# Optimization experiments

Hardware: AMD Instinct MI355X
Metric: run time of the kernel (lower is better)

## Reference

```python
import jax, jax.numpy as jnp
import numpy as np

K = 7          # involution kernel size
G = 16         # groups = channels // group_channels = 256 // 16
BN_EPS = 1e-3  # Keras BatchNormalization default epsilon


def setup_inputs() -> dict:
    key = jax.random.key(0)
    ks = jax.random.split(key, 6)
    B, H, W, C = 4, 56, 56, 256
    Cr = C // 4                      # reduction_ratio = 4
    x = jax.random.normal(ks[0], (B, H, W, C), dtype=jnp.float32)
    w_reduce = jax.random.normal(ks[1], (C, Cr), dtype=jnp.float32) * (1.0 / np.sqrt(C))
    gamma = jnp.ones((Cr,), dtype=jnp.float32)
    beta = jnp.zeros((Cr,), dtype=jnp.float32)
    mean = jax.random.normal(ks[2], (Cr,), dtype=jnp.float32) * 0.1
    var = jax.random.uniform(ks[3], (Cr,), dtype=jnp.float32) + 0.5
    w_span = jax.random.normal(ks[4], (Cr, K * K * G), dtype=jnp.float32) * (1.0 / np.sqrt(Cr))
    b_span = jnp.zeros((K * K * G,), dtype=jnp.float32)
    return {"x": x, "w_reduce": w_reduce, "gamma": gamma, "beta": beta,
            "mean": mean, "var": var, "w_span": w_span, "b_span": b_span}


def reference(x, w_reduce, gamma, beta, mean, var, w_span, b_span):
    B, H, W, C = x.shape
    Cg = C // G  # channels per group
    # kernel generation branch: 1x1 conv -> BN (inference) -> ReLU -> 1x1 conv
    r = jnp.einsum('bhwc,cd->bhwd', x, w_reduce)
    r = jax.nn.relu((r - mean) * (gamma / jnp.sqrt(var + BN_EPS)) + beta)
    kgen = jnp.einsum('bhwd,de->bhwe', r, w_span) + b_span      # (B,H,W,K*K*G)
    kgen = kgen.reshape(B, H, W, G, K * K)
    # im2col with SAME padding (stride=1, pad (K-1)//2 symmetric), depth order (kh, kw, C)
    p = (K - 1) // 2
    xp = jnp.pad(x, ((0, 0), (p, p), (p, p), (0, 0)))
    patches = jnp.stack([xp[:, i:i + H, j:j + W, :]
                         for i in range(K) for j in range(K)], axis=3)  # (B,H,W,K*K,C)
    patches = patches.reshape(B, H, W, K * K, G, Cg)
    # per-pixel, per-group weighted reduction over the K*K window
    out = jnp.einsum('bhwgk,bhwkgc->bhwgc', kgen, patches)
    return out.reshape(B, H, W, C)
```

## Files before the change

### kernel.cpp

```cpp
#include <hip/hip_runtime.h>
#include <hip/hip_bf16.h>
#include <stdint.h>

#define B_   4
#define H_   56
#define W_   56
#define C_   256
#define CR   64
#define G_   16
#define CG   16
#define KS   7
#define KK   49
#define PADR 3
#define NPX  (B_*H_*W_)

typedef __attribute__((ext_vector_type(8))) short bf16x8;
typedef __attribute__((ext_vector_type(4))) float f32x4;
typedef __attribute__((ext_vector_type(2))) float f32x2;

__device__ __forceinline__ uint32_t f2bf(float f) {
    uint32_t x = __float_as_uint(f);
    return (x + 0x7fffu + ((x >> 16) & 1u)) >> 16;
}
__device__ __forceinline__ uint32_t pkbf(float a, float b) {
    union { __hip_bfloat162 h; uint32_t u; } c;
    c.h = __float22bfloat162_rn(make_float2(a, b));
    return c.u;
}
__device__ __forceinline__ float blo(uint32_t w) { return __uint_as_float(w << 16); }
__device__ __forceinline__ float bhi(uint32_t w) { return __uint_as_float(w & 0xffff0000u); }

union U4V { uint4 u; bf16x8 v; };

__global__ __launch_bounds__(256) void k0_prepack(
        const float* __restrict__ wr, const float* __restrict__ wspan,
        const float* __restrict__ gamma, const float* __restrict__ beta,
        const float* __restrict__ mean, const float* __restrict__ var,
        uint16_t* __restrict__ wrp, uint16_t* __restrict__ wpp,
        float* __restrict__ scale, float* __restrict__ shift) {
    int idx = blockIdx.x * 256 + threadIdx.x;
    {
        int j = idx & 7, lane = (idx >> 3) & 63, nb = (idx >> 9) & 3,
            kb = (idx >> 11) & 1, g = idx >> 12;
        int k = kb * 32 + (lane >> 4) * 8 + j;
        int n = nb * 16 + (lane & 15);
        float v = (n < KK) ? wspan[k * (KK * G_) + g * KK + n] : 0.f;
        wpp[idx] = (uint16_t)f2bf(v);
    }
    if (idx < 16384) {
        int j = idx & 7, lane = (idx >> 3) & 63, nb = (idx >> 9) & 3, kb = idx >> 11;
        int k = kb * 32 + (lane >> 4) * 8 + j;
        int n = nb * 16 + (lane & 15);
        wrp[idx] = (uint16_t)f2bf(wr[k * CR + n]);
    }
    if (idx < CR) {
        float s = gamma[idx] * rsqrtf(var[idx] + 1e-3f);
        scale[idx] = s;
        shift[idx] = beta[idx] - mean[idx] * s;
    }
}

__global__ __launch_bounds__(256) void k1_reduce(
        const float* __restrict__ x, const uint16_t* __restrict__ wrp,
        const float* __restrict__ scale, const float* __restrict__ shift,
        uint16_t* __restrict__ r) {
    int tid = threadIdx.x;
    int lane = tid & 63, w = tid >> 6;
    int mt = blockIdx.x * 4 + w;
    int pix = mt * 16 + (lane & 15);
    int ko = (lane >> 4) * 8;
    const float* xrow = x + (size_t)pix * C_ + ko;

    float s4[4], sh4[4];
    #pragma unroll
    for (int nb = 0; nb < 4; ++nb) {
        int d = nb * 16 + (lane & 15);
        s4[nb] = scale[d];
        sh4[nb] = shift[d];
    }

    float4 a0[8], a1[8];
    #pragma unroll
    for (int kb = 0; kb < 8; ++kb) {
        a0[kb] = *(const float4*)(xrow + kb * 32);
        a1[kb] = *(const float4*)(xrow + kb * 32 + 4);
    }
    f32x4 acc[4] = {{0,0,0,0},{0,0,0,0},{0,0,0,0},{0,0,0,0}};
    #pragma unroll
    for (int kb = 0; kb < 8; ++kb) {
        U4V af;
        af.u = make_uint4(pkbf(a0[kb].x, a0[kb].y), pkbf(a0[kb].z, a0[kb].w),
                          pkbf(a1[kb].x, a1[kb].y), pkbf(a1[kb].z, a1[kb].w));
        const uint16_t* wb = wrp + kb * 2048 + lane * 8;
        #pragma unroll
        for (int nb = 0; nb < 4; ++nb) {
            bf16x8 bf_ = *(const bf16x8*)(wb + nb * 512);
            acc[nb] = __builtin_amdgcn_mfma_f32_16x16x32_bf16(af.v, bf_, acc[nb], 0, 0, 0);
        }
    }
    int rq = (lane >> 4) * 4;
    #pragma unroll
    for (int nb = 0; nb < 4; ++nb) {
        #pragma unroll
        for (int rg = 0; rg < 4; ++rg) {
            float v = fmaf(acc[nb][rg], s4[nb], sh4[nb]);
            v = v > 0.f ? v : 0.f;
            r[(size_t)(mt * 16 + rq + rg) * CR + (nb * 16 + (lane & 15))] = (uint16_t)f2bf(v);
        }
    }
}

#define TS   14
#define HS   20
#define XSP  21
#define KGW  56

__global__ __launch_bounds__(256, 4) void k2_involution(
        const float* __restrict__ x, const uint16_t* __restrict__ r,
        const uint16_t* __restrict__ wpp, const float* __restrict__ bspan,
        float* __restrict__ out) {
    __shared__ __align__(16) uint16_t xs[420 * 16];
    __shared__ __align__(16) uint16_t kg[196 * KGW];

    int tid  = threadIdx.x;
    int tile = blockIdx.x, g = blockIdx.y, b = blockIdx.z;
    int ty0 = (tile >> 2) * TS, tx0 = (tile & 3) * TS;
    int lane = tid & 63, w = tid >> 6;

    bf16x8 bfr[2][4];
    const uint16_t* wb = wpp + g * 4096 + lane * 8;
    #pragma unroll
    for (int kb = 0; kb < 2; ++kb)
        #pragma unroll
        for (int nb = 0; nb < 4; ++nb)
            bfr[kb][nb] = *(const bf16x8*)(wb + kb * 2048 + nb * 512);
    float bias[4];
    #pragma unroll
    for (int nb = 0; nb < 4; ++nb) {
        int n = nb * 16 + (lane & 15);
        bias[nb] = (n < KK) ? bspan[g * KK + n] : 0.f;
    }

    #pragma unroll
    for (int pass = 0; pass < 2; ++pass) {
        int i = tid + pass * 256;
        if (i < HS * HS) {
            int py = i / HS, px = i % HS;
            int gy = ty0 + py - PADR, gx = tx0 + px - PADR;
            uint4 wA = make_uint4(0, 0, 0, 0), wB = wA;
            if (gy >= 0 && gy < H_ && gx >= 0 && gx < W_) {
                const float* xp = x + (((size_t)(b * H_ + gy)) * W_ + gx) * C_ + g * CG;
                float4 q0 = *(const float4*)(xp);
                float4 q1 = *(const float4*)(xp + 4);
                float4 q2 = *(const float4*)(xp + 8);
                float4 q3 = *(const float4*)(xp + 12);
                wA = make_uint4(pkbf(q0.x, q0.y), pkbf(q0.z, q0.w),
                                pkbf(q1.x, q1.y), pkbf(q1.z, q1.w));
                wB = make_uint4(pkbf(q2.x, q2.y), pkbf(q2.z, q2.w),
                                pkbf(q3.x, q3.y), pkbf(q3.z, q3.w));
            }
            uint16_t* dst = xs + (py * XSP + px) * 16;
            *(uint4*)(dst + 0) = wA;
            *(uint4*)(dst + 8) = wB;
        }
    }

    bf16x8 ra[4][2];
    #pragma unroll
    for (int mi = 0; mi < 4; ++mi) {
        int mt = mi * 4 + w;
        int mtc = mt < 13 ? mt : 12;
        int m  = mtc * 16 + (lane & 15);
        int mm = m < 196 ? m : 195;
        int ly = mm / TS, lx = mm % TS;
        size_t pix = ((size_t)(b * H_ + ty0 + ly)) * W_ + (tx0 + lx);
        const uint16_t* rp = r + pix * CR + (lane >> 4) * 8;
        ra[mi][0] = *(const bf16x8*)(rp);
        ra[mi][1] = *(const bf16x8*)(rp + 32);
    }
    #pragma unroll
    for (int mi = 0; mi < 4; ++mi) {
        int mt = mi * 4 + w;
        if (mt < 13) {
            f32x4 acc[4];
            #pragma unroll
            for (int nb = 0; nb < 4; ++nb)
                acc[nb] = (f32x4){bias[nb], bias[nb], bias[nb], bias[nb]};
            #pragma unroll
            for (int nb = 0; nb < 4; ++nb) {
                acc[nb] = __builtin_amdgcn_mfma_f32_16x16x32_bf16(ra[mi][0], bfr[0][nb], acc[nb], 0, 0, 0);
                acc[nb] = __builtin_amdgcn_mfma_f32_16x16x32_bf16(ra[mi][1], bfr[1][nb], acc[nb], 0, 0, 0);
            }
            int row = mt * 16 + (lane >> 4) * 4;
            if (row < 196) {
                #pragma unroll
                for (int nb = 0; nb < 4; ++nb) {
                    int n = nb * 16 + (lane & 15);
                    if (n < KK) {
                        int slot = n + n / 7;
                        #pragma unroll
                        for (int rg = 0; rg < 4; ++rg) {
                            int rr  = row + rg;
                            int rho = (rr >> 1) + (rr & 1) * 98;
                            kg[rho * KGW + slot] = (uint16_t)f2bf(acc[nb][rg]);
                        }
                    }
                }
            }
        }
    }
    __syncthreads();

    if (tid < 196) {
        int p = tid >> 1, h = tid & 1;
        int ty = p / 7, tx = (p % 7) * 2;
        const uint16_t* kgL = kg + p * KGW;
        const uint16_t* kgR = kg + (98 + p) * KGW;

        f32x2 accL[4] = {{0,0},{0,0},{0,0},{0,0}};
        f32x2 accR[4] = {{0,0},{0,0},{0,0},{0,0}};
        #pragma unroll
        for (int kh = 0; kh < KS; ++kh) {
            uint4 aL = *(const uint4*)(kgL + kh * 8);
            uint4 aR = *(const uint4*)(kgR + kh * 8);
            const uint32_t kwL[4] = {aL.x, aL.y, aL.z, aL.w};
            const uint32_t kwR[4] = {aR.x, aR.y, aR.z, aR.w};
            const uint16_t* xrow = xs + ((ty + kh) * XSP + tx) * 16 + h * 8;
            #pragma unroll
            for (int j = 0; j < 8; ++j) {
                uint4 xw = *(const uint4*)(xrow + j * 16);
                float kvL = 0.f, kvR = 0.f;
                if (j < 7) kvL = (j & 1) ? bhi(kwL[j >> 1]) : blo(kwL[j >> 1]);
                if (j > 0) { int t = j - 1; kvR = (t & 1) ? bhi(kwR[t >> 1]) : blo(kwR[t >> 1]); }
                f32x2 kL = {kvL, kvL}, kR = {kvR, kvR};
                f32x2 x0 = {blo(xw.x), bhi(xw.x)};
                f32x2 x1 = {blo(xw.y), bhi(xw.y)};
                f32x2 x2 = {blo(xw.z), bhi(xw.z)};
                f32x2 x3 = {blo(xw.w), bhi(xw.w)};
                accL[0] = __builtin_elementwise_fma(kL, x0, accL[0]);
                accL[1] = __builtin_elementwise_fma(kL, x1, accL[1]);
                accL[2] = __builtin_elementwise_fma(kL, x2, accL[2]);
                accL[3] = __builtin_elementwise_fma(kL, x3, accL[3]);
                accR[0] = __builtin_elementwise_fma(kR, x0, accR[0]);
                accR[1] = __builtin_elementwise_fma(kR, x1, accR[1]);
                accR[2] = __builtin_elementwise_fma(kR, x2, accR[2]);
                accR[3] = __builtin_elementwise_fma(kR, x3, accR[3]);
            }
        }
        size_t pixL = ((size_t)(b * H_ + ty0 + ty)) * W_ + (tx0 + tx);
        float* opL = out + pixL * C_ + g * CG + h * 8;
        float* opR = opL + C_;
        *(float4*)(opL + 0) = make_float4(accL[0].x, accL[0].y, accL[1].x, accL[1].y);
        *(float4*)(opL + 4) = make_float4(accL[2].x, accL[2].y, accL[3].x, accL[3].y);
        *(float4*)(opR + 0) = make_float4(accR[0].x, accR[0].y, accR[1].x, accR[1].y);
        *(float4*)(opR + 4) = make_float4(accR[2].x, accR[2].y, accR[3].x, accR[3].y);
    }
}

extern "C" void kernel_launch(void* const* d_in, const int* in_sizes, int n_in,
                              void* d_out, int out_size, void* d_ws, size_t ws_size,
                              hipStream_t stream) {
    const float* x        = (const float*)d_in[0];
    const float* w_reduce = (const float*)d_in[1];
    const float* gamma    = (const float*)d_in[2];
    const float* beta     = (const float*)d_in[3];
    const float* mean     = (const float*)d_in[4];
    const float* var      = (const float*)d_in[5];
    const float* w_span   = (const float*)d_in[6];
    const float* b_span   = (const float*)d_in[7];
    float* out = (float*)d_out;

    uint8_t* ws = (uint8_t*)d_ws;
    uint16_t* r_ws  = (uint16_t*)(ws + 0);
    uint16_t* wrp   = (uint16_t*)(ws + 1605632);
    uint16_t* wpp   = (uint16_t*)(ws + 1638400);
    float*    scale = (float*)   (ws + 1769472);
    float*    shift = (float*)   (ws + 1769728);

    hipLaunchKernelGGL(k0_prepack, dim3(256), dim3(256), 0, stream,
                       w_reduce, w_span, gamma, beta, mean, var,
                       wrp, wpp, scale, shift);
    hipLaunchKernelGGL(k1_reduce, dim3(NPX / 64), dim3(256), 0, stream,
                       x, wrp, scale, shift, r_ws);
    hipLaunchKernelGGL(k2_involution, dim3(16, 16, B_), dim3(256), 0, stream,
                       x, r_ws, wpp, b_span, out);
}
```

Baseline: 98.67 us.

## Fuse prepack, reduce and involution kernels into one persistent launch with grid barriers

Merges the three kernels into a single 1024-block launch. Atomic-counter grid barriers separate the weight prepack, the reduction GEMM and the involution phases, and a magic value in workspace handles one-time counter initialisation. The goal is to remove launch gaps and per-kernel tails between the stages. The cost is that only one wave in five does reduce work, so that phase runs with less parallelism. The scheme also depends on all 1024 blocks being co-resident (4 per CU at 256 CUs), and a barrier deadlock is possible if occupancy falls short.

```diff
diff --git a/kernel.cpp b/kernel.cpp
--- a/kernel.cpp
+++ b/kernel.cpp
@@ -13,6 +13,8 @@
 #define KK   49
 #define PADR 3
 #define NPX  (B_*H_*W_)
+#define NBLK 1024
+#define MAGIC 0x9E37C0DE13572468ull
 
 typedef __attribute__((ext_vector_type(8))) short bf16x8;
 typedef __attribute__((ext_vector_type(4))) float f32x4;
@@ -32,82 +34,14 @@
 
 union U4V { uint4 u; bf16x8 v; };
 
-__global__ __launch_bounds__(256) void k0_prepack(
-        const float* __restrict__ wr, const float* __restrict__ wspan,
-        const float* __restrict__ gamma, const float* __restrict__ beta,
-        const float* __restrict__ mean, const float* __restrict__ var,
-        uint16_t* __restrict__ wrp, uint16_t* __restrict__ wpp,
-        float* __restrict__ scale, float* __restrict__ shift) {
-    int idx = blockIdx.x * 256 + threadIdx.x;
-    {
-        int j = idx & 7, lane = (idx >> 3) & 63, nb = (idx >> 9) & 3,
-            kb = (idx >> 11) & 1, g = idx >> 12;
-        int k = kb * 32 + (lane >> 4) * 8 + j;
-        int n = nb * 16 + (lane & 15);
-        float v = (n < KK) ? wspan[k * (KK * G_) + g * KK + n] : 0.f;
-        wpp[idx] = (uint16_t)f2bf(v);
-    }
-    if (idx < 16384) {
-        int j = idx & 7, lane = (idx >> 3) & 63, nb = (idx >> 9) & 3, kb = idx >> 11;
-        int k = kb * 32 + (lane >> 4) * 8 + j;
-        int n = nb * 16 + (lane & 15);
-        wrp[idx] = (uint16_t)f2bf(wr[k * CR + n]);
-    }
-    if (idx < CR) {
-        float s = gamma[idx] * rsqrtf(var[idx] + 1e-3f);
-        scale[idx] = s;
-        shift[idx] = beta[idx] - mean[idx] * s;
-    }
-}
-
-__global__ __launch_bounds__(256) void k1_reduce(
-        const float* __restrict__ x, const uint16_t* __restrict__ wrp,
-        const float* __restrict__ scale, const float* __restrict__ shift,
-        uint16_t* __restrict__ r) {
-    int tid = threadIdx.x;
-    int lane = tid & 63, w = tid >> 6;
-    int mt = blockIdx.x * 4 + w;
-    int pix = mt * 16 + (lane & 15);
-    int ko = (lane >> 4) * 8;
-    const float* xrow = x + (size_t)pix * C_ + ko;
-
-    float s4[4], sh4[4];
-    #pragma unroll
-    for (int nb = 0; nb < 4; ++nb) {
-        int d = nb * 16 + (lane & 15);
-        s4[nb] = scale[d];
-        sh4[nb] = shift[d];
-    }
-
-    float4 a0[8], a1[8];
-    #pragma unroll
-    for (int kb = 0; kb < 8; ++kb) {
-        a0[kb] = *(const float4*)(xrow + kb * 32);
-        a1[kb] = *(const float4*)(xrow + kb * 32 + 4);
-    }
-    f32x4 acc[4] = {{0,0,0,0},{0,0,0,0},{0,0,0,0},{0,0,0,0}};
-    #pragma unroll
-    for (int kb = 0; kb < 8; ++kb) {
-        U4V af;
-        af.u = make_uint4(pkbf(a0[kb].x, a0[kb].y), pkbf(a0[kb].z, a0[kb].w),
-                          pkbf(a1[kb].x, a1[kb].y), pkbf(a1[kb].z, a1[kb].w));
-        const uint16_t* wb = wrp + kb * 2048 + lane * 8;
-        #pragma unroll
-        for (int nb = 0; nb < 4; ++nb) {
-            bf16x8 bf_ = *(const bf16x8*)(wb + nb * 512);
-            acc[nb] = __builtin_amdgcn_mfma_f32_16x16x32_bf16(af.v, bf_, acc[nb], 0, 0, 0);
-        }
-    }
-    int rq = (lane >> 4) * 4;
-    #pragma unroll
-    for (int nb = 0; nb < 4; ++nb) {
-        #pragma unroll
-        for (int rg = 0; rg < 4; ++rg) {
-            float v = fmaf(acc[nb][rg], s4[nb], sh4[nb]);
-            v = v > 0.f ? v : 0.f;
-            r[(size_t)(mt * 16 + rq + rg) * CR + (nb * 16 + (lane & 15))] = (uint16_t)f2bf(v);
-        }
-    }
+__device__ __forceinline__ void gbar(uint32_t* c, int tid) {
+    __syncthreads();
+    if (tid == 0) {
+        __hip_atomic_fetch_add(c, 1u, __ATOMIC_ACQ_REL, __HIP_MEMORY_SCOPE_AGENT);
+        while (__hip_atomic_load(c, __ATOMIC_ACQUIRE, __HIP_MEMORY_SCOPE_AGENT) < (uint32_t)NBLK)
+            __builtin_amdgcn_s_sleep(2);
+    }
+    __syncthreads();
 }
 
 #define TS   14
@@ -115,25 +49,113 @@
 #define XSP  21
 #define KGW  56
 
-__global__ __launch_bounds__(256, 4) void k2_involution(
-        const float* __restrict__ x, const uint16_t* __restrict__ r,
-        const uint16_t* __restrict__ wpp, const float* __restrict__ bspan,
-        float* __restrict__ out) {
+__global__ __launch_bounds__(256, 4) void k_all(
+        const float* __restrict__ x, const float* __restrict__ wr,
+        const float* __restrict__ wspan,
+        const float* __restrict__ gamma, const float* __restrict__ beta,
+        const float* __restrict__ mean, const float* __restrict__ var,
+        const float* __restrict__ bspan,
+        uint16_t* __restrict__ r, uint16_t* __restrict__ wrp,
+        uint16_t* __restrict__ wpp, float* __restrict__ scale,
+        float* __restrict__ shift, uint8_t* sync, float* __restrict__ out) {
     __shared__ __align__(16) uint16_t xs[420 * 16];
     __shared__ __align__(16) uint16_t kg[196 * KGW];
 
     int tid  = threadIdx.x;
-    int tile = blockIdx.x, g = blockIdx.y, b = blockIdx.z;
+    int bid  = blockIdx.x;
+    int lane = tid & 63, w = tid >> 6;
+
+    if (w == 0) {
+        int idx = bid * 64 + lane;
+        int j = idx & 7, fl = (idx >> 3) & 63, nb = (idx >> 9) & 3,
+            kb = (idx >> 11) & 1, g = idx >> 12;
+        int k = kb * 32 + (fl >> 4) * 8 + j;
+        int n = nb * 16 + (fl & 15);
+        float v = (n < KK) ? wspan[k * (KK * G_) + g * KK + n] : 0.f;
+        wpp[idx] = (uint16_t)f2bf(v);
+    } else if (w == 1 && bid < 256) {
+        int idx = bid * 64 + lane;
+        int j = idx & 7, fl = (idx >> 3) & 63, nb = (idx >> 9) & 3, kb = idx >> 11;
+        int k = kb * 32 + (fl >> 4) * 8 + j;
+        int n = nb * 16 + (fl & 15);
+        wrp[idx] = (uint16_t)f2bf(wr[k * CR + n]);
+    } else if (w == 2 && bid == 0) {
+        float s = gamma[lane] * rsqrtf(var[lane] + 1e-3f);
+        scale[lane] = s;
+        shift[lane] = beta[lane] - mean[lane] * s;
+    }
+
+    uint64_t* magic = (uint64_t*)sync;
+    uint32_t* ctr   = (uint32_t*)(sync + 8);
+    if (tid == 0) {
+        if (bid == 0) {
+            if (__hip_atomic_load(magic, __ATOMIC_ACQUIRE, __HIP_MEMORY_SCOPE_AGENT) != MAGIC) {
+                __hip_atomic_store(&ctr[0], 0u, __ATOMIC_RELAXED, __HIP_MEMORY_SCOPE_AGENT);
+                __hip_atomic_store(&ctr[1], 0u, __ATOMIC_RELAXED, __HIP_MEMORY_SCOPE_AGENT);
+                __hip_atomic_store(&ctr[2], 0u, __ATOMIC_RELAXED, __HIP_MEMORY_SCOPE_AGENT);
+                __hip_atomic_store(magic, (uint64_t)MAGIC, __ATOMIC_RELEASE, __HIP_MEMORY_SCOPE_AGENT);
+            }
+        } else {
+            while (__hip_atomic_load(magic, __ATOMIC_ACQUIRE, __HIP_MEMORY_SCOPE_AGENT) != MAGIC)
+                __builtin_amdgcn_s_sleep(2);
+        }
+    }
+    gbar(&ctr[0], tid);
+
+    {
+        int gw = bid * 4 + w;
+        if (gw < 3920 && gw % 5 == 0) {
+            int mt  = gw / 5;
+            int pix = mt * 16 + (lane & 15);
+            int ko  = (lane >> 4) * 8;
+            const float* xrow = x + (size_t)pix * C_ + ko;
+            float s4[4], sh4[4];
+            #pragma unroll
+            for (int nb = 0; nb < 4; ++nb) {
+                int d = nb * 16 + (lane & 15);
+                s4[nb] = scale[d];
+                sh4[nb] = shift[d];
+            }
+            f32x4 acc[4] = {{0,0,0,0},{0,0,0,0},{0,0,0,0},{0,0,0,0}};
+            #pragma unroll
+            for (int kb = 0; kb < 8; ++kb) {
+                float4 a0 = *(const float4*)(xrow + kb * 32);
+                float4 a1 = *(const float4*)(xrow + kb * 32 + 4);
+                U4V af;
+                af.u = make_uint4(pkbf(a0.x, a0.y), pkbf(a0.z, a0.w),
+                                  pkbf(a1.x, a1.y), pkbf(a1.z, a1.w));
+                const uint16_t* wb = wrp + kb * 2048 + lane * 8;
+                #pragma unroll
+                for (int nb = 0; nb < 4; ++nb) {
+                    bf16x8 bf_ = *(const bf16x8*)(wb + nb * 512);
+                    acc[nb] = __builtin_amdgcn_mfma_f32_16x16x32_bf16(af.v, bf_, acc[nb], 0, 0, 0);
+                }
+            }
+            int rq = (lane >> 4) * 4;
+            #pragma unroll
+            for (int nb = 0; nb < 4; ++nb) {
+                #pragma unroll
+                for (int rg = 0; rg < 4; ++rg) {
+                    float v = fmaf(acc[nb][rg], s4[nb], sh4[nb]);
+                    v = v > 0.f ? v : 0.f;
+                    r[(size_t)(mt * 16 + rq + rg) * CR + (nb * 16 + (lane & 15))] =
+                        (uint16_t)f2bf(v);
+                }
+            }
+        }
+    }
+    gbar(&ctr[1], tid);
+
+    int tile = bid & 15, g = (bid >> 4) & 15, b = bid >> 8;
     int ty0 = (tile >> 2) * TS, tx0 = (tile & 3) * TS;
-    int lane = tid & 63, w = tid >> 6;
 
     bf16x8 bfr[2][4];
-    const uint16_t* wb = wpp + g * 4096 + lane * 8;
+    const uint16_t* wb2 = wpp + g * 4096 + lane * 8;
     #pragma unroll
     for (int kb = 0; kb < 2; ++kb)
         #pragma unroll
         for (int nb = 0; nb < 4; ++nb)
-            bfr[kb][nb] = *(const bf16x8*)(wb + kb * 2048 + nb * 512);
+            bfr[kb][nb] = *(const bf16x8*)(wb2 + kb * 2048 + nb * 512);
     float bias[4];
     #pragma unroll
     for (int nb = 0; nb < 4; ++nb) {
@@ -255,6 +277,15 @@
         *(float4*)(opR + 0) = make_float4(accR[0].x, accR[0].y, accR[1].x, accR[1].y);
         *(float4*)(opR + 4) = make_float4(accR[2].x, accR[2].y, accR[3].x, accR[3].y);
     }
+
+    if (tid == 0) {
+        uint32_t old = __hip_atomic_fetch_add(&ctr[2], 1u, __ATOMIC_ACQ_REL, __HIP_MEMORY_SCOPE_AGENT);
+        if (old == (uint32_t)(NBLK - 1)) {
+            __hip_atomic_store(&ctr[0], 0u, __ATOMIC_RELAXED, __HIP_MEMORY_SCOPE_AGENT);
+            __hip_atomic_store(&ctr[1], 0u, __ATOMIC_RELAXED, __HIP_MEMORY_SCOPE_AGENT);
+            __hip_atomic_store(&ctr[2], 0u, __ATOMIC_RELEASE, __HIP_MEMORY_SCOPE_AGENT);
+        }
+    }
 }
 
 extern "C" void kernel_launch(void* const* d_in, const int* in_sizes, int n_in,
@@ -276,12 +307,9 @@
     uint16_t* wpp   = (uint16_t*)(ws + 1638400);
     float*    scale = (float*)   (ws + 1769472);
     float*    shift = (float*)   (ws + 1769728);
-
-    hipLaunchKernelGGL(k0_prepack, dim3(256), dim3(256), 0, stream,
-                       w_reduce, w_span, gamma, beta, mean, var,
-                       wrp, wpp, scale, shift);
-    hipLaunchKernelGGL(k1_reduce, dim3(NPX / 64), dim3(256), 0, stream,
-                       x, wrp, scale, shift, r_ws);
-    hipLaunchKernelGGL(k2_involution, dim3(16, 16, B_), dim3(256), 0, stream,
-                       x, r_ws, wpp, b_span, out);
-}
+    uint8_t*  sync  = ws + 1769984;
+
+    hipLaunchKernelGGL(k_all, dim3(NBLK), dim3(256), 0, stream,
+                       x, w_reduce, w_span, gamma, beta, mean, var, b_span,
+                       r_ws, wrp, wpp, scale, shift, sync, out);
+}
```

New measurement: 310.7 us. +214.8%, slower.
